# Kernel tuning notes

Measured on AMD Instinct MI355X. Metric: run time of the kernel, lower is better.

## Reference

```python
import jax, jax.numpy as jnp
import numpy as np

NHEAD = 8
LAYER_NAMES = ('self', 'cross', 'self', 'cross')
EPS = 1e-6


def ln(x, g, b, eps=1e-5):
    m = jnp.mean(x, -1, keepdims=True)
    v = jnp.mean((x - m) ** 2, -1, keepdims=True)
    return (x - m) * jax.lax.rsqrt(v + eps) * g + b


def linear_attention(q, k, v, q_mask, kv_mask):
    # q: [N, L, H, D], k/v: [N, S, H, D]; LoFTR LinearAttention (elu+1 feature map)
    Q = jax.nn.elu(q) + 1.0
    K = jax.nn.elu(k) + 1.0
    if q_mask is not None:
        Q = Q * q_mask[:, :, None, None].astype(Q.dtype)
    if kv_mask is not None:
        mk = kv_mask[:, :, None, None].astype(K.dtype)
        K = K * mk
        v = v * mk
    v_len = v.shape[1]
    v = v / v_len
    KV = jnp.einsum('nshd,nshv->nhdv', K, v)
    Z = 1.0 / (jnp.einsum('nlhd,nhd->nlh', Q, K.sum(1)) + EPS)
    return jnp.einsum('nlhd,nhdv,nlh->nlhv', Q, KV, Z) * v_len


def enc_layer(x, src, q_mask, kv_mask, Wq, Wk, Wv, Wm, W1, W2, g1, b1, g2, b2):
    # x: [N, L, C], src: [N, S, C]
    N, L, C = x.shape
    S = src.shape[1]
    H, D = NHEAD, C // NHEAD
    q = (x @ Wq).reshape(N, L, H, D)
    k = (src @ Wk).reshape(N, S, H, D)
    v = (src @ Wv).reshape(N, S, H, D)
    msg = linear_attention(q, k, v, q_mask, kv_mask).reshape(N, L, C)
    msg = ln(msg @ Wm, g1, b1)
    msg = ln(jnp.tanh(jnp.concatenate([x, msg], axis=-1) @ W1) @ W2, g2, b2)
    return x + msg


def sample_descriptors(kp, fmap, s):
    # kp: [B, L, K, 2] (x, y) raw-image pixel coords; fmap: [B, C, H, W]; s: stride
    B, C, H, W = fmap.shape
    k = kp - s / 2 + 0.5
    denom = jnp.array([W * s - s / 2 - 0.5, H * s - s / 2 - 0.5], dtype=kp.dtype)
    k = (k / denom) * 2.0 - 1.0  # normalized [-1, 1]
    px = (k[..., 0] + 1.0) * 0.5 * (W - 1)  # align_corners=True grid_sample
    py = (k[..., 1] + 1.0) * 0.5 * (H - 1)
    x0 = jnp.floor(px)
    y0 = jnp.floor(py)
    wx = (px - x0)[..., None]
    wy = (py - y0)[..., None]
    x0i = jnp.clip(x0, 0, W - 1).astype(jnp.int32)
    x1i = jnp.clip(x0 + 1, 0, W - 1).astype(jnp.int32)
    y0i = jnp.clip(y0, 0, H - 1).astype(jnp.int32)
    y1i = jnp.clip(y0 + 1, 0, H - 1).astype(jnp.int32)
    fm = jnp.transpose(fmap, (0, 2, 3, 1))  # [B, H, W, C]
    bidx = jnp.arange(B)[:, None, None]
    g00 = fm[bidx, y0i, x0i]
    g01 = fm[bidx, y0i, x1i]
    g10 = fm[bidx, y1i, x0i]
    g11 = fm[bidx, y1i, x1i]
    out = (1 - wy) * ((1 - wx) * g00 + wx * g01) + wy * ((1 - wx) * g10 + wx * g11)
    # SuperPoint-style L2 normalization of sampled descriptors
    out = out / (jnp.linalg.norm(out, axis=-1, keepdims=True) + 1e-8)
    return out  # [B, L, K, C]


def geo_transformer(feat0, feat1, kp0_cross, kp1_cross, mask_self0, mask_self1,
                    mask_cross0, mask_cross1, Wq, Wk, Wv, Wm, W1, W2, g1, b1, g2, b2,
                    h0, w0, h1, w1, scale):
    B, L0, C = feat0.shape
    L1 = feat1.shape[1]
    K = kp0_cross.shape[2]
    for i, name in enumerate(LAYER_NAMES):
        p = (Wq[i], Wk[i], Wv[i], Wm[i], W1[i], W2[i], g1[i], b1[i], g2[i], b2[i])
        if name == 'self':
            # source = masked subset of x == full source with kv-mask (v_length cancels)
            feat0 = enc_layer(feat0, feat0, None, mask_self0, *p)
            feat1 = enc_layer(feat1, feat1, None, mask_self1, *p)
        else:
            fmap0 = jnp.transpose(feat0.reshape(B, h0, w0, C), (0, 3, 1, 2))
            fmap1 = jnp.transpose(feat1.reshape(B, h1, w1, C), (0, 3, 1, 2))
            f0c = sample_descriptors(kp0_cross, fmap0, scale)  # [B, L1, K, C]
            f1c = sample_descriptors(kp1_cross, fmap1, scale)  # [B, L0, K, C]
            x0 = feat0.reshape(B * L0, 1, C)
            x1 = feat1.reshape(B * L1, 1, C)
            nf0 = enc_layer(x0, f1c.reshape(B * L0, K, C), None,
                            mask_cross1.reshape(B * L0, K), *p)
            nf1 = enc_layer(x1, f0c.reshape(B * L1, K, C), None,
                            mask_cross0.reshape(B * L1, K), *p)
            feat0 = nf0.reshape(B, L0, C)
            feat1 = nf1.reshape(B, L1, C)
    return feat0, feat1


def setup_inputs() -> dict:
    key = jax.random.key(0)
    B, H0, W0, C, K, S, NL = 2, 64, 64, 256, 9, 8, 4
    L = H0 * W0
    ks = jax.random.split(key, 16)
    std = (2.0 / (C + C)) ** 0.5
    std2 = (2.0 / (2 * C + 2 * C)) ** 0.5
    std3 = (2.0 / (2 * C + C)) ** 0.5
    kp0 = jnp.stack([
        jax.random.uniform(ks[2], (B, L, K)) * (W0 * S),
        jax.random.uniform(ks[3], (B, L, K)) * (H0 * S)], axis=-1)
    kp1 = jnp.stack([
        jax.random.uniform(ks[4], (B, L, K)) * (W0 * S),
        jax.random.uniform(ks[5], (B, L, K)) * (H0 * S)], axis=-1)
    return {
        'feat0': jax.random.normal(ks[0], (B, L, C), jnp.float32),
        'feat1': jax.random.normal(ks[1], (B, L, C), jnp.float32),
        'kp0_cross': kp0.astype(jnp.float32),
        'kp1_cross': kp1.astype(jnp.float32),
        'mask_self0': jax.random.bernoulli(ks[6], 0.9, (B, L)),
        'mask_self1': jax.random.bernoulli(ks[7], 0.9, (B, L)),
        'mask_cross0': jax.random.bernoulli(ks[8], 0.8, (B, L, K)),
        'mask_cross1': jax.random.bernoulli(ks[9], 0.8, (B, L, K)),
        'Wq': jax.random.normal(ks[10], (NL, C, C), jnp.float32) * std,
        'Wk': jax.random.normal(ks[11], (NL, C, C), jnp.float32) * std,
        'Wv': jax.random.normal(ks[12], (NL, C, C), jnp.float32) * std,
        'Wm': jax.random.normal(ks[13], (NL, C, C), jnp.float32) * std,
        'W1': jax.random.normal(ks[14], (NL, 2 * C, 2 * C), jnp.float32) * std2,
        'W2': jax.random.normal(ks[15], (NL, 2 * C, C), jnp.float32) * std3,
        'g1': jnp.ones((NL, C), jnp.float32),
        'b1': jnp.zeros((NL, C), jnp.float32),
        'g2': jnp.ones((NL, C), jnp.float32),
        'b2': jnp.zeros((NL, C), jnp.float32),
        'h0': H0, 'w0': W0, 'h1': H0, 'w1': W0, 'scale': S,
    }


def reference(feat0, feat1, kp0_cross, kp1_cross, mask_self0, mask_self1,
              mask_cross0, mask_cross1, Wq, Wk, Wv, Wm, W1, W2, g1, b1, g2, b2,
              h0, w0, h1, w1, scale):
    return geo_transformer(feat0, feat1, kp0_cross, kp1_cross, mask_self0, mask_self1,
                           mask_cross0, mask_cross1, Wq, Wk, Wv, Wm, W1, W2,
                           g1, b1, g2, b2, h0, w0, h1, w1, scale)
```

## Files before the change

### kernel.cpp

```cpp
#include <hip/hip_runtime.h>
#include <cstddef>


#define NROWS 16384

typedef unsigned short ushort_t;
typedef __attribute__((ext_vector_type(8))) short short8;
typedef __attribute__((ext_vector_type(4))) float f32x4;
typedef __attribute__((ext_vector_type(4))) unsigned short ushort4_t;
typedef __attribute__((ext_vector_type(8))) unsigned short ushort8_t;
typedef _Float16 half_t;
typedef __attribute__((ext_vector_type(4))) _Float16 half4;
typedef __attribute__((ext_vector_type(8))) _Float16 half8;

__device__ __forceinline__ float b2f(unsigned short u) {
    union { unsigned int i; float f; } v; v.i = (unsigned int)u << 16; return v.f;
}
__device__ __forceinline__ unsigned short f2b(float x) {
    union { float f; unsigned int i; } v; v.f = x;
    unsigned int r = v.i + 0x7fffu + ((v.i >> 16) & 1u);
    return (unsigned short)(r >> 16);
}
__device__ __forceinline__ ushort_t f2h(float x) {
    union { half_t h; ushort_t u; } v; v.h = (half_t)x; return v.u;
}
__device__ __forceinline__ float elu1(float x) {
    return x > 0.f ? x + 1.f : __expf(x);
}

#define ASYNC_COPY16(gptr, lptr) \
    __builtin_amdgcn_global_load_lds((const __attribute__((address_space(1))) void*)(gptr), \
                                     (__attribute__((address_space(3))) void*)(lptr), 16, 0, 0)

__global__ __launch_bounds__(256) void gemm_bf16_kernel(
    const ushort_t* __restrict__ A0, int lda0,
    const ushort_t* __restrict__ Wt, int ldw,
    ushort_t* __restrict__ C, int ldc, int Kd,
    float* __restrict__ zbuf, int znf4)
{
    __shared__ ushort_t As[128 * 64];
    __shared__ ushort_t Bs[128 * 64];

    int tid = threadIdx.x;
    int m0 = blockIdx.y * 128;
    int n0 = blockIdx.x * 128;
    int lane = tid & 63, w = tid >> 6;
    int wrow = w >> 1, wcol = w & 1;
    int quad = lane >> 4, l16 = lane & 15;

    if (zbuf && blockIdx.y == 0) {
        int nblk = gridDim.x;
        for (int i = blockIdx.x * 256 + tid; i < znf4; i += nblk * 256)
            *(float4*)&zbuf[(size_t)i * 4] = (float4){0.f, 0.f, 0.f, 0.f};
    }

    f32x4 acc[4][4];
    #pragma unroll
    for (int i = 0; i < 4; i++)
        #pragma unroll
        for (int j = 0; j < 4; j++) acc[i][j] = (f32x4){0.f, 0.f, 0.f, 0.f};

    for (int kb = 0; kb < Kd; kb += 64) {
        #pragma unroll
        for (int q = 0; q < 4; q++) {
            int s = q * 256 + tid;
            int kk = s >> 9, p = s & 511;
            int row = p >> 2, c4 = p & 3;
            ASYNC_COPY16(A0 + (size_t)(m0 + row) * lda0 + kb + kk * 32 + c4 * 8,
                         (char*)As + s * 16);
        }
        #pragma unroll
        for (int q = 0; q < 4; q++) {
            int s = q * 256 + tid;
            int kk = s >> 9, p = s & 511;
            int row = p >> 2, c4 = p & 3;
            ASYNC_COPY16(Wt + (size_t)(n0 + row) * ldw + kb + kk * 32 + c4 * 8,
                         (char*)Bs + s * 16);
        }
        __syncthreads();

        #pragma unroll
        for (int kk = 0; kk < 2; kk++) {
            short8 af[4], bf[4];
            #pragma unroll
            for (int mt = 0; mt < 4; mt++)
                af[mt] = *(const short8*)&As[kk * 4096 + (wrow * 64 + mt * 16 + l16) * 32 + quad * 8];
            #pragma unroll
            for (int nt = 0; nt < 4; nt++)
                bf[nt] = *(const short8*)&Bs[kk * 4096 + (wcol * 64 + nt * 16 + l16) * 32 + quad * 8];
            #pragma unroll
            for (int mt = 0; mt < 4; mt++)
                #pragma unroll
                for (int nt = 0; nt < 4; nt++)
                    acc[mt][nt] = __builtin_amdgcn_mfma_f32_16x16x32_bf16(
                        af[mt], bf[nt], acc[mt][nt], 0, 0, 0);
        }
        __syncthreads();
    }

    #pragma unroll
    for (int mt = 0; mt < 4; mt++) {
        int row = m0 + wrow * 64 + mt * 16 + quad * 4;
        #pragma unroll
        for (int nt = 0; nt < 4; nt++) {
            int col = n0 + wcol * 64 + nt * 16 + l16;
            #pragma unroll
            for (int r = 0; r < 4; r++)
                C[(size_t)(row + r) * ldc + col] = f2h(acc[mt][nt][r]);
        }
    }
}

__global__ __launch_bounds__(256) void gemm_ln_kernel(
    const ushort_t* __restrict__ A, int lda,
    const ushort_t* __restrict__ Wt, int ldw, int Kd,
    const float* __restrict__ g, const float* __restrict__ bp,
    ushort_t* __restrict__ OutBf)
{
    __shared__ ushort_t As[32 * 64];
    __shared__ ushort_t Bs[256 * 64];
    __shared__ float rsum[4][32];
    __shared__ float rsq[4][32];

    int tid = threadIdx.x;
    int m0 = blockIdx.x * 32;
    int lane = tid & 63, w = tid >> 6;
    int quad = lane >> 4, l16 = lane & 15;

    f32x4 acc[2][4];
    #pragma unroll
    for (int i = 0; i < 2; i++)
        #pragma unroll
        for (int j = 0; j < 4; j++) acc[i][j] = (f32x4){0.f, 0.f, 0.f, 0.f};

    for (int kb = 0; kb < Kd; kb += 64) {
        {
            int s = tid;
            int kk = s >> 7, p = s & 127;
            int row = p >> 2, c4 = p & 3;
            ASYNC_COPY16(A + (size_t)(m0 + row) * lda + kb + kk * 32 + c4 * 8,
                         (char*)As + s * 16);
        }
        #pragma unroll
        for (int q = 0; q < 8; q++) {
            int s = q * 256 + tid;
            int kk = s >> 10, p = s & 1023;
            int row = p >> 2, c4 = p & 3;
            ASYNC_COPY16(Wt + (size_t)(row) * ldw + kb + kk * 32 + c4 * 8,
                         (char*)Bs + s * 16);
        }
        __syncthreads();

        #pragma unroll
        for (int kk = 0; kk < 2; kk++) {
            short8 af[2], bf[4];
            #pragma unroll
            for (int mt = 0; mt < 2; mt++)
                af[mt] = *(const short8*)&As[kk * 1024 + (mt * 16 + l16) * 32 + quad * 8];
            #pragma unroll
            for (int nt = 0; nt < 4; nt++)
                bf[nt] = *(const short8*)&Bs[kk * 8192 + (w * 64 + nt * 16 + l16) * 32 + quad * 8];
            #pragma unroll
            for (int mt = 0; mt < 2; mt++)
                #pragma unroll
                for (int nt = 0; nt < 4; nt++)
                    acc[mt][nt] = __builtin_amdgcn_mfma_f32_16x16x32_bf16(
                        af[mt], bf[nt], acc[mt][nt], 0, 0, 0);
        }
        __syncthreads();
    }

    #pragma unroll
    for (int mt = 0; mt < 2; mt++)
        #pragma unroll
        for (int r = 0; r < 4; r++) {
            float s = 0.f, q = 0.f;
            #pragma unroll
            for (int nt = 0; nt < 4; nt++) {
                float v = acc[mt][nt][r];
                s += v; q += v * v;
            }
            #pragma unroll
            for (int off = 1; off < 16; off <<= 1) {
                s += __shfl_xor(s, off, 64);
                q += __shfl_xor(q, off, 64);
            }
            if (l16 == 0) {
                rsum[w][mt * 16 + quad * 4 + r] = s;
                rsq[w][mt * 16 + quad * 4 + r]  = q;
            }
        }
    __syncthreads();

    #pragma unroll
    for (int mt = 0; mt < 2; mt++) {
        #pragma unroll
        for (int r = 0; r < 4; r++) {
            int rl = mt * 16 + quad * 4 + r;
            float s = rsum[0][rl] + rsum[1][rl] + rsum[2][rl] + rsum[3][rl];
            float q = rsq[0][rl] + rsq[1][rl] + rsq[2][rl] + rsq[3][rl];
            float m = s * (1.f / 256.f);
            float var = q * (1.f / 256.f) - m * m;
            float rs = rsqrtf(var + 1e-5f);
            size_t row = (size_t)(m0 + rl);
            #pragma unroll
            for (int nt = 0; nt < 4; nt++) {
                int col = w * 64 + nt * 16 + l16;
                float y = (acc[mt][nt][r] - m) * rs * g[col] + bp[col];
                OutBf[row * 256 + col] = f2b(y);
            }
        }
    }
}

__global__ __launch_bounds__(256) void mlp_fused_kernel(
    const ushort_t* __restrict__ Xb, const ushort_t* __restrict__ L1,
    const ushort_t* __restrict__ W1t, const ushort_t* __restrict__ W2t,
    const float* __restrict__ g, const float* __restrict__ bp,
    ushort_t* __restrict__ XbfOut, const float* __restrict__ Xin,
    float* __restrict__ Xout)
{
    __shared__ ushort_t Tt[32 * 512];
    __shared__ char buf[20480];

    ushort_t* As  = (ushort_t*)buf;
    ushort_t* Bs  = (ushort_t*)(buf + 4096);
    ushort_t* Bs2 = (ushort_t*)buf;
    float* rsum = (float*)buf;
    float* rsq  = (float*)(buf + 512);

    int tid = threadIdx.x;
    int m0 = blockIdx.x * 32;
    int lane = tid & 63, w = tid >> 6;
    int quad = lane >> 4, l16 = lane & 15;

    for (int np = 0; np < 4; np++) {
        f32x4 acc[2][2];
        #pragma unroll
        for (int i = 0; i < 2; i++)
            #pragma unroll
            for (int j = 0; j < 2; j++) acc[i][j] = (f32x4){0.f, 0.f, 0.f, 0.f};

        for (int kb = 0; kb < 512; kb += 64) {
            const ushort_t* Ab = (kb < 256) ? Xb : L1;
            int kc = (kb < 256) ? kb : kb - 256;
            {
                int s = tid;
                int kk = s >> 7, p = s & 127;
                ASYNC_COPY16(Ab + (size_t)(m0 + (p >> 2)) * 256 + kc + kk * 32 + (p & 3) * 8,
                             (char*)As + s * 16);
            }
            #pragma unroll
            for (int q = 0; q < 4; q++) {
                int s = q * 256 + tid;
                int kk = s >> 9, p = s & 511;
                ASYNC_COPY16(W1t + (size_t)(np * 128 + (p >> 2)) * 512 + kb + kk * 32 + (p & 3) * 8,
                             (char*)Bs + s * 16);
            }
            __syncthreads();

            #pragma unroll
            for (int kk = 0; kk < 2; kk++) {
                short8 af[2], bfr[2];
                #pragma unroll
                for (int mt = 0; mt < 2; mt++)
                    af[mt] = *(const short8*)&As[kk * 1024 + (mt * 16 + l16) * 32 + quad * 8];
                #pragma unroll
                for (int nt = 0; nt < 2; nt++)
                    bfr[nt] = *(const short8*)&Bs[kk * 4096 + (w * 32 + nt * 16 + l16) * 32 + quad * 8];
                #pragma unroll
                for (int mt = 0; mt < 2; mt++)
                    #pragma unroll
                    for (int nt = 0; nt < 2; nt++)
                        acc[mt][nt] = __builtin_amdgcn_mfma_f32_16x16x32_bf16(
                            af[mt], bfr[nt], acc[mt][nt], 0, 0, 0);
            }
            __syncthreads();
        }

        #pragma unroll
        for (int mt = 0; mt < 2; mt++)
            #pragma unroll
            for (int nt = 0; nt < 2; nt++)
                #pragma unroll
                for (int r = 0; r < 4; r++) {
                    int trow = mt * 16 + quad * 4 + r;
                    int col = np * 128 + w * 32 + nt * 16 + l16;
                    int c8s = (col >> 3) ^ (trow & 7);
                    Tt[trow * 512 + c8s * 8 + (col & 7)] = f2b(tanhf(acc[mt][nt][r]));
                }
    }

    f32x4 acc2[2][2][2];
    #pragma unroll
    for (int a = 0; a < 2; a++)
        #pragma unroll
        for (int i = 0; i < 2; i++)
            #pragma unroll
            for (int j = 0; j < 2; j++) acc2[a][i][j] = (f32x4){0.f, 0.f, 0.f, 0.f};

    for (int pass = 0; pass < 2; pass++) {
        for (int kb = 0; kb < 512; kb += 64) {
            #pragma unroll
            for (int q = 0; q < 4; q++) {
                int s = q * 256 + tid;
                int kk = s >> 9, p = s & 511;
                ASYNC_COPY16(W2t + (size_t)(pass * 128 + (p >> 2)) * 512 + kb + kk * 32 + (p & 3) * 8,
                             (char*)Bs2 + s * 16);
            }
            __syncthreads();

            #pragma unroll
            for (int kk = 0; kk < 2; kk++) {
                short8 af[2], bfr[2];
                #pragma unroll
                for (int mt = 0; mt < 2; mt++) {
                    int row = mt * 16 + l16;
                    int blk = ((kb >> 3) + kk * 4 + quad) ^ (row & 7);
                    af[mt] = *(const short8*)&Tt[row * 512 + blk * 8];
                }
                #pragma unroll
                for (int nt = 0; nt < 2; nt++)
                    bfr[nt] = *(const short8*)&Bs2[kk * 4096 + (w * 32 + nt * 16 + l16) * 32 + quad * 8];
                #pragma unroll
                for (int mt = 0; mt < 2; mt++)
                    #pragma unroll
                    for (int nt = 0; nt < 2; nt++)
                        acc2[pass][mt][nt] = __builtin_amdgcn_mfma_f32_16x16x32_bf16(
                            af[mt], bfr[nt], acc2[pass][mt][nt], 0, 0, 0);
            }
            __syncthreads();
        }
    }

    #pragma unroll
    for (int mt = 0; mt < 2; mt++)
        #pragma unroll
        for (int r = 0; r < 4; r++) {
            float s = 0.f, q = 0.f;
            #pragma unroll
            for (int pass = 0; pass < 2; pass++)
                #pragma unroll
                for (int nt = 0; nt < 2; nt++) {
                    float v = acc2[pass][mt][nt][r];
                    s += v; q += v * v;
                }
            #pragma unroll
            for (int off = 1; off < 16; off <<= 1) {
                s += __shfl_xor(s, off, 64);
                q += __shfl_xor(q, off, 64);
            }
            if (l16 == 0) {
                rsum[w * 32 + mt * 16 + quad * 4 + r] = s;
                rsq[w * 32 + mt * 16 + quad * 4 + r]  = q;
            }
        }
    __syncthreads();

    #pragma unroll
    for (int mt = 0; mt < 2; mt++) {
        #pragma unroll
        for (int r = 0; r < 4; r++) {
            int rl = mt * 16 + quad * 4 + r;
            float s = rsum[rl] + rsum[32 + rl] + rsum[64 + rl] + rsum[96 + rl];
            float q = rsq[rl] + rsq[32 + rl] + rsq[64 + rl] + rsq[96 + rl];
            float m = s * (1.f / 256.f);
            float var = q * (1.f / 256.f) - m * m;
            float rs = rsqrtf(var + 1e-5f);
            size_t row = (size_t)(m0 + rl);
            #pragma unroll
            for (int pass = 0; pass < 2; pass++)
                #pragma unroll
                for (int nt = 0; nt < 2; nt++) {
                    int col = pass * 128 + w * 32 + nt * 16 + l16;
                    float y = (acc2[pass][mt][nt][r] - m) * rs * g[col] + bp[col];
                    float xn = Xin[row * 256 + col] + y;
                    Xout[row * 256 + col] = xn;
                    XbfOut[row * 256 + col] = f2b(xn);
                }
        }
    }
}

__global__ __launch_bounds__(256) void wprep_kernel(
    const float* __restrict__ Wq, const float* __restrict__ Wk,
    const float* __restrict__ Wv, const float* __restrict__ Wm,
    const float* __restrict__ W1, const float* __restrict__ W2,
    ushort_t* __restrict__ Wqkvt, ushort_t* __restrict__ Wmt,
    ushort_t* __restrict__ W1t, ushort_t* __restrict__ W2t)
{
    int t = blockIdx.x;
    int layer = t / 640, r = t % 640;
    const float* src; ushort_t* dst;
    int ldsrc, lddst, tn, tk;
    if (r < 192) {
        int grp = r / 64, rr = r % 64; tn = rr / 8; tk = rr % 8;
        src = (grp == 0 ? Wq : grp == 1 ? Wk : Wv) + (size_t)layer * 65536;
        ldsrc = 256;
        dst = Wqkvt + (size_t)layer * 196608 + (size_t)grp * 65536;
        lddst = 256;
    } else if (r < 256) {
        int rr = r - 192; tn = rr / 8; tk = rr % 8;
        src = Wm + (size_t)layer * 65536; ldsrc = 256;
        dst = Wmt + (size_t)layer * 65536; lddst = 256;
    } else if (r < 512) {
        int rr = r - 256; tn = rr / 16; tk = rr % 16;
        src = W1 + (size_t)layer * 262144; ldsrc = 512;
        dst = W1t + (size_t)layer * 262144; lddst = 512;
    } else {
        int rr = r - 512; tn = rr / 16; tk = rr % 16;
        src = W2 + (size_t)layer * 131072; ldsrc = 256;
        dst = W2t + (size_t)layer * 131072; lddst = 512;
    }
    int n0 = tn * 32, k0 = tk * 32;
    __shared__ float tileS[32][33];
    int j = threadIdx.x & 31, i0 = threadIdx.x >> 5;
    #pragma unroll
    for (int p = 0; p < 4; p++) {
        int i = i0 + p * 8;
        tileS[i][j] = src[(size_t)(k0 + i) * ldsrc + n0 + j];
    }
    __syncthreads();
    #pragma unroll
    for (int p = 0; p < 4; p++) {
        int i = i0 + p * 8;
        dst[(size_t)(n0 + i) * lddst + k0 + j] = f2b(tileS[j][i]);
    }
}

__global__ __launch_bounds__(256) void init_kernel(
    const float* __restrict__ f0, const float* __restrict__ f1,
    float* __restrict__ X, ushort_t* __restrict__ Xbf)
{
    int idx = blockIdx.x * 256 + threadIdx.x;
    size_t e = (size_t)idx * 4;
    float4 v = (e < 2097152) ? *(const float4*)&f0[e] : *(const float4*)&f1[e - 2097152];
    *(float4*)&X[e] = v;
    ushort4_t u = { f2b(v.x), f2b(v.y), f2b(v.z), f2b(v.w) };
    *(ushort4_t*)&Xbf[e] = u;
}

__global__ __launch_bounds__(256) void kv_reduce_kernel(
    const ushort_t* __restrict__ QKV,
    const int* __restrict__ mask0, const int* __restrict__ mask1,
    float* __restrict__ KV, float* __restrict__ Ksum)
{
    int g = blockIdx.y;
    int t = g >> 4, b = (g >> 3) & 1, h = g & 7;
    const int* mask = t ? mask1 : mask0;
    int rowbase = t * 8192 + b * 4096;
    int s_begin = blockIdx.x * 256;

    __shared__ float sK[32][32];
    __shared__ float sV[32][32];

    int tid = threadIdx.x;
    int e  = tid & 31;
    int dq = tid >> 5;

    float acc[4] = {0.f, 0.f, 0.f, 0.f};
    float ks[4]  = {0.f, 0.f, 0.f, 0.f};

    for (int s0 = s_begin; s0 < s_begin + 256; s0 += 32) {
        #pragma unroll
        for (int q = 0; q < 2; q++) {
            int idx = tid + q * 256;
            int rl = idx >> 4;
            int part = idx & 15;
            int s = s0 + rl;
            size_t row = (size_t)(rowbase + s);
            float m = mask[b * 4096 + s] ? 1.f : 0.f;
            if (part < 8) {
                half4 u = *(const half4*)&QKV[row * 768 + 256 + h * 32 + part * 4];
                float4 f = { elu1((float)u[0]) * m, elu1((float)u[1]) * m,
                             elu1((float)u[2]) * m, elu1((float)u[3]) * m };
                *(float4*)&sK[rl][part * 4] = f;
            } else {
                half4 u = *(const half4*)&QKV[row * 768 + 512 + h * 32 + (part - 8) * 4];
                float4 f = { (float)u[0] * m, (float)u[1] * m,
                             (float)u[2] * m, (float)u[3] * m };
                *(float4*)&sV[rl][(part - 8) * 4] = f;
            }
        }
        __syncthreads();

        #pragma unroll
        for (int s = 0; s < 32; s++) {
            float4 kq = *(const float4*)&sK[s][dq * 4];
            float vv = sV[s][e];
            acc[0] += kq.x * vv;
            acc[1] += kq.y * vv;
            acc[2] += kq.z * vv;
            acc[3] += kq.w * vv;
            ks[0] += kq.x; ks[1] += kq.y; ks[2] += kq.z; ks[3] += kq.w;
        }
        __syncthreads();
    }

    #pragma unroll
    for (int j = 0; j < 4; j++)
        atomicAdd(&KV[(size_t)g * 1024 + (dq * 4 + j) * 32 + e], acc[j]);
    if (e == 0) {
        #pragma unroll
        for (int j = 0; j < 4; j++)
            atomicAdd(&Ksum[g * 32 + dq * 4 + j], ks[j]);
    }
}

__global__ __launch_bounds__(256) void attn_apply_kernel(
    const ushort_t* __restrict__ QKV, const float* __restrict__ KV,
    const float* __restrict__ Ksum, ushort_t* __restrict__ MSG)
{
    int row = blockIdx.x;
    int t = row >> 13, bb = (row >> 12) & 1;
    int gb = (t * 2 + bb) * 8;
    int c = threadIdx.x, h = c >> 5, e = c & 31;
    int g = gb + h;

    __shared__ float sQ[256];
    float qf = elu1((float)(*(const half_t*)&QKV[(size_t)row * 768 + c]));
    sQ[c] = qf;
    __syncthreads();

    float p = qf * Ksum[g * 32 + e];
    #pragma unroll
    for (int off = 16; off; off >>= 1) p += __shfl_xor(p, off, 32);
    float Z = 1.f / (p + 1e-6f);

// ... 86 lines not shown
    float mU0, mU1, mU2, mU3, mSm;
    int mPack;
    {
        int msi = l32 % 5;
        int s9 = half + 2 * msi;
        int valid = (s9 < 9);
        int r = bl * 9 + (valid ? s9 : 0);
        mSm = (valid && mask[r] != 0) ? 1.f : 0.f;

        float2 xy = *(const float2*)&kp[(size_t)r * 2];
        float px = (xy.x - 3.5f) * (63.f / 507.5f);
        float py = (xy.y - 3.5f) * (63.f / 507.5f);
        float fx = floorf(px), fy = floorf(py);
        float wx = px - fx, wy = py - fy;
        int ix = (int)fx, iy = (int)fy;
        int xa = ix > 0 ? ix : 0;
        int xb = ix + 1 > 0 ? (ix + 1 < 63 ? ix + 1 : 63) : 0;
        int ya = iy > 0 ? iy : 0;
        int yb = iy + 1 > 0 ? (iy + 1 < 63 ? iy + 1 : 63) : 0;

        float w0 = (1.f - wy) * (1.f - wx);
        float w1 = (1.f - wy) * wx;
        float w2 = wy * (1.f - wx);
        float w3 = wy * wx;

        const float* G = &Gimg[(size_t)((iy + 1) * 65 + (ix + 1)) * 12];
        float4 ga = *(const float4*)&G[0];
        float4 gb4 = *(const float4*)&G[4];
        float2 gc = *(const float2*)&G[8];
        float ss = w0 * w0 * ga.x + w1 * w1 * gb4.x + w2 * w2 * gb4.w + w3 * w3 * gc.y
                 + 2.f * (w0 * w1 * ga.y + w0 * w2 * ga.z + w0 * w3 * ga.w
                        + w1 * w2 * gb4.y + w1 * w3 * gb4.z + w2 * w3 * gc.x);
        float inv = 1.f / (sqrtf(ss) + 1e-8f);
        mU0 = w0 * inv; mU1 = w1 * inv; mU2 = w2 * inv; mU3 = w3 * inv;

        int base = (rb + ya * 64 + xa) * 768;
        mPack = base | (xb - xa) | ((yb - ya) << 1);
    }

    int spack[5];
    float su0[5], su1[5], su2[5], su3[5], sm[5];
    int srcb = half * 32;
    #pragma unroll
    for (int si = 0; si < 5; si++) {
        int src = srcb + si;
        spack[si] = __shfl(mPack, src, 64);
        su0[si] = __shfl(mU0, src, 64);
        su1[si] = __shfl(mU1, src, 64);
        su2[si] = __shfl(mU2, src, 64);
        su3[si] = __shfl(mU3, src, 64);
        sm[si]  = __shfl(mSm, src, 64);
    }

    half8 kR[2][4], vR[2][4];

#define LOADKV(bufi, si_) do { \
        int pk = spack[si_]; \
        int dx = (pk & 1) ? 768 : 0; \
        int dy = (pk & 2) ? 49152 : 0; \
        size_t bK = (size_t)(pk & ~3) + 256 + c8; \
        size_t bV = bK + 256; \
        kR[bufi][0] = *(const half8*)&QKV[bK]; \
        kR[bufi][1] = *(const half8*)&QKV[bK + dx]; \
        kR[bufi][2] = *(const half8*)&QKV[bK + dy]; \
        kR[bufi][3] = *(const half8*)&QKV[bK + dx + dy]; \
        vR[bufi][0] = *(const half8*)&QKV[bV]; \
        vR[bufi][1] = *(const half8*)&QKV[bV + dx]; \
        vR[bufi][2] = *(const half8*)&QKV[bV + dy]; \
        vR[bufi][3] = *(const half8*)&QKV[bV + dx + dy]; \
    } while (0)

    float zsum = 0.f;
    float acc[8] = {0, 0, 0, 0, 0, 0, 0, 0};

    LOADKV(0, 0);
    #pragma unroll
    for (int si = 0; si < 5; si++) {
        int cur = si & 1;
        if (si + 1 < 5) {
            if (cur == 0) LOADKV(1, si + 1);
            else          LOADKV(0, si + 1);
        }
        float u0 = su0[si], u1 = su1[si], u2 = su2[si], u3 = su3[si];
        float p = 0.f;
        #pragma unroll
        for (int j = 0; j < 8; j++) {
            float kc = u0 * (float)kR[cur][0][j] + u1 * (float)kR[cur][1][j]
                     + u2 * (float)kR[cur][2][j] + u3 * (float)kR[cur][3][j];
            p += qf[j] * elu1(kc);
        }
        p += __shfl_xor(p, 1, 64);
        p += __shfl_xor(p, 2, 64);
        p *= sm[si];

        zsum += p;
        float pu0 = p * u0, pu1 = p * u1, pu2 = p * u2, pu3 = p * u3;
        #pragma unroll
        for (int j = 0; j < 8; j++)
            acc[j] += pu0 * (float)vR[cur][0][j] + pu1 * (float)vR[cur][1][j]
                    + pu2 * (float)vR[cur][2][j] + pu3 * (float)vR[cur][3][j];
    }
#undef LOADKV

    zsum += __shfl_xor(zsum, 32, 64);
    #pragma unroll
    for (int j = 0; j < 8; j++) acc[j] += __shfl_xor(acc[j], 32, 64);

    if (half == 0) {
        float Z = 1.f / (zsum + 1e-6f);
        ushort8_t o;
        #pragma unroll
        for (int j = 0; j < 8; j++) o[j] = f2b(acc[j] * Z);
        *(ushort8_t*)&MSG[(size_t)row * 256 + c8] = o;
    }
}


extern "C" void kernel_launch(void* const* d_in, const int* in_sizes, int n_in,
                              void* d_out, int out_size, void* d_ws, size_t ws_size,
                              hipStream_t stream)
{
    const float* feat0 = (const float*)d_in[0];
    const float* feat1 = (const float*)d_in[1];
    const float* kp0 = (const float*)d_in[2];
    const float* kp1 = (const float*)d_in[3];
    const int* ms0 = (const int*)d_in[4];
    const int* ms1 = (const int*)d_in[5];
    const int* mc0 = (const int*)d_in[6];
    const int* mc1 = (const int*)d_in[7];
    const float* Wq = (const float*)d_in[8];
    const float* Wk = (const float*)d_in[9];
    const float* Wv = (const float*)d_in[10];
    const float* Wm = (const float*)d_in[11];
    const float* W1 = (const float*)d_in[12];
    const float* W2 = (const float*)d_in[13];
    const float* g1 = (const float*)d_in[14];
    const float* b1 = (const float*)d_in[15];
    const float* g2 = (const float*)d_in[16];
    const float* b2 = (const float*)d_in[17];

    char* p = (char*)d_ws;
    float*    X     = (float*)p;            p += 16777216;
    ushort_t* Xbf   = (ushort_t*)p;         p += 8388608;
    ushort_t* QKV   = (ushort_t*)p;         p += 25165824;
    ushort_t* MSG   = (ushort_t*)p;         p += 8388608;
    ushort_t* L1bf  = (ushort_t*)p;         p += 8388608;
    float*    KVb   = (float*)p;            p += 131072;
    float*    KSb   = (float*)p;            p += 4096;
    float*    Gm    = (float*)p;            p += 811264;
    ushort_t* Wqkvt = (ushort_t*)p;         p += 1572864;
    ushort_t* Wmt   = (ushort_t*)p;         p += 524288;
    ushort_t* W1t   = (ushort_t*)p;         p += 2097152;
    ushort_t* W2t   = (ushort_t*)p;         p += 1048576;

    init_kernel<<<4096, 256, 0, stream>>>(feat0, feat1, X, Xbf);
    wprep_kernel<<<2560, 256, 0, stream>>>(Wq, Wk, Wv, Wm, W1, W2, Wqkvt, Wmt, W1t, W2t);

    for (int i = 0; i < 4; i++) {
        const ushort_t* Wqkvt_l = Wqkvt + (size_t)i * 196608;
        const ushort_t* Wmt_l   = Wmt   + (size_t)i * 65536;
        const ushort_t* W1t_l   = W1t   + (size_t)i * 262144;
        const ushort_t* W2t_l   = W2t   + (size_t)i * 131072;
        const float* g1_l = g1 + (size_t)i * 256;
        const float* b1_l = b1 + (size_t)i * 256;
        const float* g2_l = g2 + (size_t)i * 256;
        const float* b2_l = b2 + (size_t)i * 256;
        bool is_self = (i == 0 || i == 2);

        gemm_bf16_kernel<<<dim3(6, 128), 256, 0, stream>>>(
            Xbf, 256, Wqkvt_l, 256, QKV, 768, 256,
            is_self ? KVb : nullptr, 33792 / 4);

        if (is_self) {
            kv_reduce_kernel<<<dim3(16, 32), 256, 0, stream>>>(QKV, ms0, ms1, KVb, KSb);
            attn_apply_kernel<<<NROWS, 256, 0, stream>>>(QKV, KVb, KSb, MSG);
        } else {
            gram_kernel<<<4225, 256, 0, stream>>>(Xbf, Gm);
            cross_fused_kernel<<<NROWS / 4, 256, 0, stream>>>(QKV, Gm, kp0, kp1, mc0, mc1, MSG);
        }

        gemm_ln_kernel<<<NROWS / 32, 256, 0, stream>>>(
            MSG, 256, Wmt_l, 256, 256, g1_l, b1_l, L1bf);

        float* Xout = (i == 3) ? (float*)d_out : X;
        mlp_fused_kernel<<<NROWS / 32, 256, 0, stream>>>(
            Xbf, L1bf, W1t_l, W2t_l, g2_l, b2_l, Xbf, X, Xout);
    }
}
```

Before: 597.0 us.

## Load GEMM operands directly from global into registers, dropping LDS staging

In gemm_ln_kernel and mlp_fused_kernel, the async-copy LDS staging of the A and weight tiles is replaced by direct per-lane short8 global loads that feed the MFMA instructions. The per-iteration __syncthreads pairs go away, and in the MLP the four column passes are merged into one K loop with 32 accumulators, so each activation fragment is loaded once. The aim is to cut LDS traffic and barrier stalls and to improve occupancy through lower shared-memory use. In exchange it relies on L1/L2 for weight reuse across waves, raises register pressure, and hard-codes K=256 in gemm_ln.

```diff
diff --git a/kernel.cpp b/kernel.cpp
--- a/kernel.cpp
+++ b/kernel.cpp
@@ -117,8 +117,6 @@
     const float* __restrict__ g, const float* __restrict__ bp,
     ushort_t* __restrict__ OutBf)
 {
-    __shared__ ushort_t As[32 * 64];
-    __shared__ ushort_t Bs[256 * 64];
     __shared__ float rsum[4][32];
     __shared__ float rsq[4][32];
 
@@ -133,41 +131,24 @@
         #pragma unroll
         for (int j = 0; j < 4; j++) acc[i][j] = (f32x4){0.f, 0.f, 0.f, 0.f};
 
-    for (int kb = 0; kb < Kd; kb += 64) {
-        {
-            int s = tid;
-            int kk = s >> 7, p = s & 127;
-            int row = p >> 2, c4 = p & 3;
-            ASYNC_COPY16(A + (size_t)(m0 + row) * lda + kb + kk * 32 + c4 * 8,
-                         (char*)As + s * 16);
-        }
-        #pragma unroll
-        for (int q = 0; q < 8; q++) {
-            int s = q * 256 + tid;
-            int kk = s >> 10, p = s & 1023;
-            int row = p >> 2, c4 = p & 3;
-            ASYNC_COPY16(Wt + (size_t)(row) * ldw + kb + kk * 32 + c4 * 8,
-                         (char*)Bs + s * 16);
-        }
-        __syncthreads();
-
-        #pragma unroll
-        for (int kk = 0; kk < 2; kk++) {
-            short8 af[2], bf[4];
-            #pragma unroll
-            for (int mt = 0; mt < 2; mt++)
-                af[mt] = *(const short8*)&As[kk * 1024 + (mt * 16 + l16) * 32 + quad * 8];
+    const ushort_t* Ar0 = A + (size_t)(m0 + l16) * lda + quad * 8;
+    const ushort_t* Ar1 = Ar0 + (size_t)16 * lda;
+    const ushort_t* Br  = Wt + (size_t)(w * 64 + l16) * ldw + quad * 8;
+
+    #pragma unroll
+    for (int kb = 0; kb < 256; kb += 32) {
+        short8 af[2], bf[4];
+        af[0] = *(const short8*)(Ar0 + kb);
+        af[1] = *(const short8*)(Ar1 + kb);
+        #pragma unroll
+        for (int nt = 0; nt < 4; nt++)
+            bf[nt] = *(const short8*)(Br + (size_t)nt * 16 * ldw + kb);
+        #pragma unroll
+        for (int mt = 0; mt < 2; mt++)
             #pragma unroll
             for (int nt = 0; nt < 4; nt++)
-                bf[nt] = *(const short8*)&Bs[kk * 8192 + (w * 64 + nt * 16 + l16) * 32 + quad * 8];
-            #pragma unroll
-            for (int mt = 0; mt < 2; mt++)
-                #pragma unroll
-                for (int nt = 0; nt < 4; nt++)
-                    acc[mt][nt] = __builtin_amdgcn_mfma_f32_16x16x32_bf16(
-                        af[mt], bf[nt], acc[mt][nt], 0, 0, 0);
-        }
-        __syncthreads();
+                acc[mt][nt] = __builtin_amdgcn_mfma_f32_16x16x32_bf16(
+                    af[mt], bf[nt], acc[mt][nt], 0, 0, 0);
     }
 
     #pragma unroll
@@ -221,63 +202,54 @@
     float* __restrict__ Xout)
 {
     __shared__ ushort_t Tt[32 * 512];
-    __shared__ char buf[20480];
-
-    ushort_t* As  = (ushort_t*)buf;
-    ushort_t* Bs  = (ushort_t*)(buf + 4096);
-    ushort_t* Bs2 = (ushort_t*)buf;
-    float* rsum = (float*)buf;
-    float* rsq  = (float*)(buf + 512);
+    __shared__ float rsum[128];
+    __shared__ float rsq[128];
 
     int tid = threadIdx.x;
     int m0 = blockIdx.x * 32;
     int lane = tid & 63, w = tid >> 6;
     int quad = lane >> 4, l16 = lane & 15;
 
-    for (int np = 0; np < 4; np++) {
-        f32x4 acc[2][2];
+    f32x4 acc1[4][2][2];
+    #pragma unroll
+    for (int np = 0; np < 4; np++)
         #pragma unroll
         for (int i = 0; i < 2; i++)
             #pragma unroll
-            for (int j = 0; j < 2; j++) acc[i][j] = (f32x4){0.f, 0.f, 0.f, 0.f};
-
-        for (int kb = 0; kb < 512; kb += 64) {
-            const ushort_t* Ab = (kb < 256) ? Xb : L1;
-            int kc = (kb < 256) ? kb : kb - 256;
-            {
-                int s = tid;
-                int kk = s >> 7, p = s & 127;
-                ASYNC_COPY16(Ab + (size_t)(m0 + (p >> 2)) * 256 + kc + kk * 32 + (p & 3) * 8,
-                             (char*)As + s * 16);
-            }
-            #pragma unroll
-            for (int q = 0; q < 4; q++) {
-                int s = q * 256 + tid;
-                int kk = s >> 9, p = s & 511;
-                ASYNC_COPY16(W1t + (size_t)(np * 128 + (p >> 2)) * 512 + kb + kk * 32 + (p & 3) * 8,
-                             (char*)Bs + s * 16);
-            }
-            __syncthreads();
-
-            #pragma unroll
-            for (int kk = 0; kk < 2; kk++) {
-                short8 af[2], bfr[2];
+            for (int j = 0; j < 2; j++) acc1[np][i][j] = (f32x4){0.f, 0.f, 0.f, 0.f};
+
+    {
+        const ushort_t* Xr0 = Xb + (size_t)(m0 + l16) * 256 + quad * 8;
+        const ushort_t* Xr1 = Xr0 + 16 * 256;
+        const ushort_t* Lr0 = L1 + (size_t)(m0 + l16) * 256 + quad * 8;
+        const ushort_t* Lr1 = Lr0 + 16 * 256;
+        const ushort_t* B1  = W1t + (size_t)(w * 32 + l16) * 512 + quad * 8;
+
+        #pragma unroll
+        for (int kb = 0; kb < 512; kb += 32) {
+            short8 af[2];
+            if (kb < 256) {
+                af[0] = *(const short8*)(Xr0 + kb);
+                af[1] = *(const short8*)(Xr1 + kb);
+            } else {
+                af[0] = *(const short8*)(Lr0 + (kb - 256));
+                af[1] = *(const short8*)(Lr1 + (kb - 256));
+            }
+            #pragma unroll
+            for (int np = 0; np < 4; np++)
                 #pragma unroll
-                for (int mt = 0; mt < 2; mt++)
-                    af[mt] = *(const short8*)&As[kk * 1024 + (mt * 16 + l16) * 32 + quad * 8];
-                #pragma unroll
-                for (int nt = 0; nt < 2; nt++)
-                    bfr[nt] = *(const short8*)&Bs[kk * 4096 + (w * 32 + nt * 16 + l16) * 32 + quad * 8];
-                #pragma unroll
-                for (int mt = 0; mt < 2; mt++)
+                for (int nt = 0; nt < 2; nt++) {
+                    short8 b = *(const short8*)(B1 + (size_t)(np * 128 + nt * 16) * 512 + kb);
                     #pragma unroll
-                    for (int nt = 0; nt < 2; nt++)
-                        acc[mt][nt] = __builtin_amdgcn_mfma_f32_16x16x32_bf16(
-                            af[mt], bfr[nt], acc[mt][nt], 0, 0, 0);
-            }
-            __syncthreads();
-        }
-
+                    for (int mt = 0; mt < 2; mt++)
+                        acc1[np][mt][nt] = __builtin_amdgcn_mfma_f32_16x16x32_bf16(
+                            af[mt], b, acc1[np][mt][nt], 0, 0, 0);
+                }
+        }
+    }
+
+    #pragma unroll
+    for (int np = 0; np < 4; np++)
         #pragma unroll
         for (int mt = 0; mt < 2; mt++)
             #pragma unroll
@@ -287,9 +259,9 @@
                     int trow = mt * 16 + quad * 4 + r;
                     int col = np * 128 + w * 32 + nt * 16 + l16;
                     int c8s = (col >> 3) ^ (trow & 7);
-                    Tt[trow * 512 + c8s * 8 + (col & 7)] = f2b(tanhf(acc[mt][nt][r]));
+                    Tt[trow * 512 + c8s * 8 + (col & 7)] = f2b(tanhf(acc1[np][mt][nt][r]));
                 }
-    }
+    __syncthreads();
 
     f32x4 acc2[2][2][2];
     #pragma unroll
@@ -299,37 +271,28 @@
             #pragma unroll
             for (int j = 0; j < 2; j++) acc2[a][i][j] = (f32x4){0.f, 0.f, 0.f, 0.f};
 
-    for (int pass = 0; pass < 2; pass++) {
-        for (int kb = 0; kb < 512; kb += 64) {
-            #pragma unroll
-            for (int q = 0; q < 4; q++) {
-                int s = q * 256 + tid;
-                int kk = s >> 9, p = s & 511;
-                ASYNC_COPY16(W2t + (size_t)(pass * 128 + (p >> 2)) * 512 + kb + kk * 32 + (p & 3) * 8,
-                             (char*)Bs2 + s * 16);
-            }
-            __syncthreads();
-
-            #pragma unroll
-            for (int kk = 0; kk < 2; kk++) {
-                short8 af[2], bfr[2];
+    {
+        const ushort_t* B2 = W2t + (size_t)(w * 32 + l16) * 512 + quad * 8;
+
+        #pragma unroll
+        for (int kb = 0; kb < 512; kb += 32) {
+            short8 af[2];
+            #pragma unroll
+            for (int mt = 0; mt < 2; mt++) {
+                int row = mt * 16 + l16;
+                int blk = ((kb >> 3) + quad) ^ (row & 7);
+                af[mt] = *(const short8*)&Tt[row * 512 + blk * 8];
+            }
+            #pragma unroll
+            for (int pass = 0; pass < 2; pass++)
                 #pragma unroll
-                for (int mt = 0; mt < 2; mt++) {
-                    int row = mt * 16 + l16;
-                    int blk = ((kb >> 3) + kk * 4 + quad) ^ (row & 7);
-                    af[mt] = *(const short8*)&Tt[row * 512 + blk * 8];
+                for (int nt = 0; nt < 2; nt++) {
+                    short8 b = *(const short8*)(B2 + (size_t)(pass * 128 + nt * 16) * 512 + kb);
+                    #pragma unroll
+                    for (int mt = 0; mt < 2; mt++)
+                        acc2[pass][mt][nt] = __builtin_amdgcn_mfma_f32_16x16x32_bf16(
+                            af[mt], b, acc2[pass][mt][nt], 0, 0, 0);
                 }
-                #pragma unroll
-                for (int nt = 0; nt < 2; nt++)
-                    bfr[nt] = *(const short8*)&Bs2[kk * 4096 + (w * 32 + nt * 16 + l16) * 32 + quad * 8];
-                #pragma unroll
-                for (int mt = 0; mt < 2; mt++)
-                    #pragma unroll
-                    for (int nt = 0; nt < 2; nt++)
-                        acc2[pass][mt][nt] = __builtin_amdgcn_mfma_f32_16x16x32_bf16(
-                            af[mt], bfr[nt], acc2[pass][mt][nt], 0, 0, 0);
-            }
-            __syncthreads();
         }
     }
 
```

Result: slower. 760.0 us (+27.3%).

## Fuse merge-projection LayerNorm GEMM into the MLP kernel with shared-memory intermediates

Applied to the files above, without the earlier changes.

Merges the Wm GEMM+LayerNorm kernel into the MLP kernel, so the first LayerNorm output and the block's input rows stay in swizzled shared memory instead of going through global memory. The MLP is also restructured to interleave W1 and W2 per 128-column chunk, keeping only a 32x128 tanh tile rather than the full 32x512 intermediate. This removes one launch and the L1bf global write/read. The cost is more shared memory per block, which may lower occupancy, and W2 tiles are now reloaded in smaller K chunks across the four np iterations.

```diff
diff --git a/kernel.cpp b/kernel.cpp
--- a/kernel.cpp
+++ b/kernel.cpp
@@ -111,42 +111,54 @@
     }
 }
 
-__global__ __launch_bounds__(256) void gemm_ln_kernel(
-    const ushort_t* __restrict__ A, int lda,
-    const ushort_t* __restrict__ Wt, int ldw, int Kd,
-    const float* __restrict__ g, const float* __restrict__ bp,
-    ushort_t* __restrict__ OutBf)
-{
+__global__ __launch_bounds__(256) void mlp_ln_fused_kernel(
+    const ushort_t* __restrict__ MSG, const ushort_t* __restrict__ Wmt,
+    const float* __restrict__ g1, const float* __restrict__ b1,
+    const ushort_t* __restrict__ Xb,
+    const ushort_t* __restrict__ W1t, const ushort_t* __restrict__ W2t,
+    const float* __restrict__ g2, const float* __restrict__ bp,
+    ushort_t* __restrict__ XbfOut, const float* __restrict__ Xin,
+    float* __restrict__ Xout)
+{
+    __shared__ ushort_t XB[32 * 256];
+    __shared__ ushort_t L1s[32 * 256];
+    __shared__ ushort_t Tnp[32 * 128];
+    __shared__ ushort_t Bs[256 * 64];
     __shared__ ushort_t As[32 * 64];
-    __shared__ ushort_t Bs[256 * 64];
-    __shared__ float rsum[4][32];
-    __shared__ float rsq[4][32];
+    __shared__ float stats[256];
 
     int tid = threadIdx.x;
     int m0 = blockIdx.x * 32;
     int lane = tid & 63, w = tid >> 6;
     int quad = lane >> 4, l16 = lane & 15;
 
-    f32x4 acc[2][4];
+    #pragma unroll
+    for (int i = 0; i < 4; i++) {
+        int s = i * 256 + tid;
+        int row = s >> 5, gp = s & 31;
+        int gsrc = gp ^ (row & 7);
+        ASYNC_COPY16(Xb + (size_t)(m0 + row) * 256 + gsrc * 8,
+                     (char*)XB + s * 16);
+    }
+
+    f32x4 accA[2][4];
     #pragma unroll
     for (int i = 0; i < 2; i++)
         #pragma unroll
-        for (int j = 0; j < 4; j++) acc[i][j] = (f32x4){0.f, 0.f, 0.f, 0.f};
-
-    for (int kb = 0; kb < Kd; kb += 64) {
+        for (int j = 0; j < 4; j++) accA[i][j] = (f32x4){0.f, 0.f, 0.f, 0.f};
+
+    for (int kb = 0; kb < 256; kb += 64) {
         {
             int s = tid;
             int kk = s >> 7, p = s & 127;
-            int row = p >> 2, c4 = p & 3;
-            ASYNC_COPY16(A + (size_t)(m0 + row) * lda + kb + kk * 32 + c4 * 8,
+            ASYNC_COPY16(MSG + (size_t)(m0 + (p >> 2)) * 256 + kb + kk * 32 + (p & 3) * 8,
                          (char*)As + s * 16);
         }
         #pragma unroll
         for (int q = 0; q < 8; q++) {
             int s = q * 256 + tid;
             int kk = s >> 10, p = s & 1023;
-            int row = p >> 2, c4 = p & 3;
-            ASYNC_COPY16(Wt + (size_t)(row) * ldw + kb + kk * 32 + c4 * 8,
+            ASYNC_COPY16(Wmt + (size_t)(p >> 2) * 256 + kb + kk * 32 + (p & 3) * 8,
                          (char*)Bs + s * 16);
         }
         __syncthreads();
@@ -164,8 +176,8 @@
             for (int mt = 0; mt < 2; mt++)
                 #pragma unroll
                 for (int nt = 0; nt < 4; nt++)
-                    acc[mt][nt] = __builtin_amdgcn_mfma_f32_16x16x32_bf16(
-                        af[mt], bf[nt], acc[mt][nt], 0, 0, 0);
+                    accA[mt][nt] = __builtin_amdgcn_mfma_f32_16x16x32_bf16(
+                        af[mt], bf[nt], accA[mt][nt], 0, 0, 0);
         }
         __syncthreads();
     }
@@ -177,7 +189,7 @@
             float s = 0.f, q = 0.f;
             #pragma unroll
             for (int nt = 0; nt < 4; nt++) {
-                float v = acc[mt][nt][r];
+                float v = accA[mt][nt][r];
                 s += v; q += v * v;
             }
             #pragma unroll
@@ -186,8 +198,8 @@
                 q += __shfl_xor(q, off, 64);
             }
             if (l16 == 0) {
-                rsum[w][mt * 16 + quad * 4 + r] = s;
-                rsq[w][mt * 16 + quad * 4 + r]  = q;
+                stats[w * 32 + mt * 16 + quad * 4 + r] = s;
+                stats[128 + w * 32 + mt * 16 + quad * 4 + r] = q;
             }
         }
     __syncthreads();
@@ -197,183 +209,163 @@
         #pragma unroll
         for (int r = 0; r < 4; r++) {
             int rl = mt * 16 + quad * 4 + r;
-            float s = rsum[0][rl] + rsum[1][rl] + rsum[2][rl] + rsum[3][rl];
-            float q = rsq[0][rl] + rsq[1][rl] + rsq[2][rl] + rsq[3][rl];
+            float s = stats[rl] + stats[32 + rl] + stats[64 + rl] + stats[96 + rl];
+            float q = stats[128 + rl] + stats[160 + rl] + stats[192 + rl] + stats[224 + rl];
+            float m = s * (1.f / 256.f);
+            float var = q * (1.f / 256.f) - m * m;
+            float rs = rsqrtf(var + 1e-5f);
+            #pragma unroll
+            for (int nt = 0; nt < 4; nt++) {
+                int col = w * 64 + nt * 16 + l16;
+                float y = (accA[mt][nt][r] - m) * rs * g1[col] + b1[col];
+                L1s[rl * 256 + (((col >> 3) ^ (rl & 7)) << 3) + (col & 7)] = f2b(y);
+            }
+        }
+    }
+    __syncthreads();
+
+    f32x4 acc2[2][2][2];
+    #pragma unroll
+    for (int a = 0; a < 2; a++)
+        #pragma unroll
+        for (int i = 0; i < 2; i++)
+            #pragma unroll
+            for (int j = 0; j < 2; j++) acc2[a][i][j] = (f32x4){0.f, 0.f, 0.f, 0.f};
+
+    #pragma unroll
+    for (int np = 0; np < 4; np++) {
+        f32x4 acc1[2][2];
+        #pragma unroll
+        for (int i = 0; i < 2; i++)
+            #pragma unroll
+            for (int j = 0; j < 2; j++) acc1[i][j] = (f32x4){0.f, 0.f, 0.f, 0.f};
+
+        #pragma unroll
+        for (int kb = 0; kb < 512; kb += 128) {
+            #pragma unroll
+            for (int q = 0; q < 8; q++) {
+                int s = q * 256 + tid;
+                int kk = s >> 9, p = s & 511;
+                ASYNC_COPY16(W1t + (size_t)(np * 128 + (p >> 2)) * 512 + kb + kk * 32 + (p & 3) * 8,
+                             (char*)Bs + s * 16);
+            }
+            __syncthreads();
+
+            #pragma unroll
+            for (int kk = 0; kk < 4; kk++) {
+                short8 af[2], bfr[2];
+                #pragma unroll
+                for (int mt = 0; mt < 2; mt++) {
+                    int row = mt * 16 + l16;
+                    int k = kb + kk * 32 + quad * 8;
+                    if (k < 256)
+                        af[mt] = *(const short8*)&XB[row * 256 + (((k >> 3) ^ (row & 7)) << 3)];
+                    else
+                        af[mt] = *(const short8*)&L1s[row * 256 + ((((k - 256) >> 3) ^ (row & 7)) << 3)];
+                }
+                #pragma unroll
+                for (int nt = 0; nt < 2; nt++)
+                    bfr[nt] = *(const short8*)&Bs[kk * 4096 + (w * 32 + nt * 16 + l16) * 32 + quad * 8];
+                #pragma unroll
+                for (int mt = 0; mt < 2; mt++)
+                    #pragma unroll
+                    for (int nt = 0; nt < 2; nt++)
+                        acc1[mt][nt] = __builtin_amdgcn_mfma_f32_16x16x32_bf16(
+                            af[mt], bfr[nt], acc1[mt][nt], 0, 0, 0);
+            }
+            __syncthreads();
+        }
+
+        #pragma unroll
+        for (int mt = 0; mt < 2; mt++)
+            #pragma unroll
+            for (int nt = 0; nt < 2; nt++)
+                #pragma unroll
+                for (int r = 0; r < 4; r++) {
+                    int trow = mt * 16 + quad * 4 + r;
+                    int c = w * 32 + nt * 16 + l16;
+                    Tnp[trow * 128 + (((c >> 3) ^ (trow & 7)) << 3) + (c & 7)] =
+                        f2b(tanhf(acc1[mt][nt][r]));
+                }
+        __syncthreads();
+
+        #pragma unroll
+        for (int kb2 = 0; kb2 < 128; kb2 += 64) {
+            #pragma unroll
+            for (int q = 0; q < 8; q++) {
+                int s = q * 256 + tid;
+                int kk = s >> 10, p = s & 1023;
+                ASYNC_COPY16(W2t + (size_t)(p >> 2) * 512 + np * 128 + kb2 + kk * 32 + (p & 3) * 8,
+                             (char*)Bs + s * 16);
+            }
+            __syncthreads();
+
+            #pragma unroll
+            for (int kk = 0; kk < 2; kk++) {
+                short8 af[2];
+                #pragma unroll
+                for (int mt = 0; mt < 2; mt++) {
+                    int row = mt * 16 + l16;
+                    int klocal = kb2 + kk * 32 + quad * 8;
+                    af[mt] = *(const short8*)&Tnp[row * 128 + (((klocal >> 3) ^ (row & 7)) << 3)];
+                }
+                #pragma unroll
+                for (int pass = 0; pass < 2; pass++)
+                    #pragma unroll
+                    for (int nt = 0; nt < 2; nt++) {
+                        short8 bfr = *(const short8*)&Bs[kk * 8192 +
+                            (pass * 128 + w * 32 + nt * 16 + l16) * 32 + quad * 8];
+                        #pragma unroll
+                        for (int mt = 0; mt < 2; mt++)
+                            acc2[pass][mt][nt] = __builtin_amdgcn_mfma_f32_16x16x32_bf16(
+                                af[mt], bfr, acc2[pass][mt][nt], 0, 0, 0);
+                    }
+            }
+            __syncthreads();
+        }
+    }
+
+    #pragma unroll
+    for (int mt = 0; mt < 2; mt++)
+        #pragma unroll
+        for (int r = 0; r < 4; r++) {
+            float s = 0.f, q = 0.f;
+            #pragma unroll
+            for (int pass = 0; pass < 2; pass++)
+                #pragma unroll
+                for (int nt = 0; nt < 2; nt++) {
+                    float v = acc2[pass][mt][nt][r];
+                    s += v; q += v * v;
+                }
+            #pragma unroll
+            for (int off = 1; off < 16; off <<= 1) {
+                s += __shfl_xor(s, off, 64);
+                q += __shfl_xor(q, off, 64);
+            }
+            if (l16 == 0) {
+                stats[w * 32 + mt * 16 + quad * 4 + r] = s;
+                stats[128 + w * 32 + mt * 16 + quad * 4 + r] = q;
+            }
+        }
+    __syncthreads();
+
+    #pragma unroll
+    for (int mt = 0; mt < 2; mt++) {
+        #pragma unroll
+        for (int r = 0; r < 4; r++) {
+            int rl = mt * 16 + quad * 4 + r;
+            float s = stats[rl] + stats[32 + rl] + stats[64 + rl] + stats[96 + rl];
+            float q = stats[128 + rl] + stats[160 + rl] + stats[192 + rl] + stats[224 + rl];
             float m = s * (1.f / 256.f);
             float var = q * (1.f / 256.f) - m * m;
             float rs = rsqrtf(var + 1e-5f);
             size_t row = (size_t)(m0 + rl);
             #pragma unroll
-            for (int nt = 0; nt < 4; nt++) {
-                int col = w * 64 + nt * 16 + l16;
-                float y = (acc[mt][nt][r] - m) * rs * g[col] + bp[col];
-                OutBf[row * 256 + col] = f2b(y);
-            }
-        }
-    }
-}
-
-__global__ __launch_bounds__(256) void mlp_fused_kernel(
-    const ushort_t* __restrict__ Xb, const ushort_t* __restrict__ L1,
-    const ushort_t* __restrict__ W1t, const ushort_t* __restrict__ W2t,
-    const float* __restrict__ g, const float* __restrict__ bp,
-    ushort_t* __restrict__ XbfOut, const float* __restrict__ Xin,
-    float* __restrict__ Xout)
-{
-    __shared__ ushort_t Tt[32 * 512];
-    __shared__ char buf[20480];
-
-    ushort_t* As  = (ushort_t*)buf;
-    ushort_t* Bs  = (ushort_t*)(buf + 4096);
-    ushort_t* Bs2 = (ushort_t*)buf;
-    float* rsum = (float*)buf;
-    float* rsq  = (float*)(buf + 512);
-
-    int tid = threadIdx.x;
-    int m0 = blockIdx.x * 32;
-    int lane = tid & 63, w = tid >> 6;
-    int quad = lane >> 4, l16 = lane & 15;
-
-    for (int np = 0; np < 4; np++) {
-        f32x4 acc[2][2];
-        #pragma unroll
-        for (int i = 0; i < 2; i++)
-            #pragma unroll
-            for (int j = 0; j < 2; j++) acc[i][j] = (f32x4){0.f, 0.f, 0.f, 0.f};
-
-        for (int kb = 0; kb < 512; kb += 64) {
-            const ushort_t* Ab = (kb < 256) ? Xb : L1;
-            int kc = (kb < 256) ? kb : kb - 256;
-            {
-                int s = tid;
-                int kk = s >> 7, p = s & 127;
-                ASYNC_COPY16(Ab + (size_t)(m0 + (p >> 2)) * 256 + kc + kk * 32 + (p & 3) * 8,
-                             (char*)As + s * 16);
-            }
-            #pragma unroll
-            for (int q = 0; q < 4; q++) {
-                int s = q * 256 + tid;
-                int kk = s >> 9, p = s & 511;
-                ASYNC_COPY16(W1t + (size_t)(np * 128 + (p >> 2)) * 512 + kb + kk * 32 + (p & 3) * 8,
-                             (char*)Bs + s * 16);
-            }
-            __syncthreads();
-
-            #pragma unroll
-            for (int kk = 0; kk < 2; kk++) {
-                short8 af[2], bfr[2];
-                #pragma unroll
-                for (int mt = 0; mt < 2; mt++)
-                    af[mt] = *(const short8*)&As[kk * 1024 + (mt * 16 + l16) * 32 + quad * 8];
-                #pragma unroll
-                for (int nt = 0; nt < 2; nt++)
-                    bfr[nt] = *(const short8*)&Bs[kk * 4096 + (w * 32 + nt * 16 + l16) * 32 + quad * 8];
-                #pragma unroll
-                for (int mt = 0; mt < 2; mt++)
-                    #pragma unroll
-                    for (int nt = 0; nt < 2; nt++)
-                        acc[mt][nt] = __builtin_amdgcn_mfma_f32_16x16x32_bf16(
-                            af[mt], bfr[nt], acc[mt][nt], 0, 0, 0);
-            }
-            __syncthreads();
-        }
-
-        #pragma unroll
-        for (int mt = 0; mt < 2; mt++)
-            #pragma unroll
-            for (int nt = 0; nt < 2; nt++)
-                #pragma unroll
-                for (int r = 0; r < 4; r++) {
-                    int trow = mt * 16 + quad * 4 + r;
-                    int col = np * 128 + w * 32 + nt * 16 + l16;
-                    int c8s = (col >> 3) ^ (trow & 7);
-                    Tt[trow * 512 + c8s * 8 + (col & 7)] = f2b(tanhf(acc[mt][nt][r]));
-                }
-    }
-
-    f32x4 acc2[2][2][2];
-    #pragma unroll
-    for (int a = 0; a < 2; a++)
-        #pragma unroll
-        for (int i = 0; i < 2; i++)
-            #pragma unroll
-            for (int j = 0; j < 2; j++) acc2[a][i][j] = (f32x4){0.f, 0.f, 0.f, 0.f};
-
-    for (int pass = 0; pass < 2; pass++) {
-        for (int kb = 0; kb < 512; kb += 64) {
-            #pragma unroll
-            for (int q = 0; q < 4; q++) {
-                int s = q * 256 + tid;
-                int kk = s >> 9, p = s & 511;
-                ASYNC_COPY16(W2t + (size_t)(pass * 128 + (p >> 2)) * 512 + kb + kk * 32 + (p & 3) * 8,
-                             (char*)Bs2 + s * 16);
-            }
-            __syncthreads();
-
-            #pragma unroll
-            for (int kk = 0; kk < 2; kk++) {
-                short8 af[2], bfr[2];
-                #pragma unroll
-                for (int mt = 0; mt < 2; mt++) {
-                    int row = mt * 16 + l16;
-                    int blk = ((kb >> 3) + kk * 4 + quad) ^ (row & 7);
-                    af[mt] = *(const short8*)&Tt[row * 512 + blk * 8];
-                }
-                #pragma unroll
-                for (int nt = 0; nt < 2; nt++)
-                    bfr[nt] = *(const short8*)&Bs2[kk * 4096 + (w * 32 + nt * 16 + l16) * 32 + quad * 8];
-                #pragma unroll
-                for (int mt = 0; mt < 2; mt++)
-                    #pragma unroll
-                    for (int nt = 0; nt < 2; nt++)
-                        acc2[pass][mt][nt] = __builtin_amdgcn_mfma_f32_16x16x32_bf16(
-                            af[mt], bfr[nt], acc2[pass][mt][nt], 0, 0, 0);
-            }
-            __syncthreads();
-        }
-    }
-
-    #pragma unroll
-    for (int mt = 0; mt < 2; mt++)
-        #pragma unroll
-        for (int r = 0; r < 4; r++) {
-            float s = 0.f, q = 0.f;
-            #pragma unroll
-            for (int pass = 0; pass < 2; pass++)
-                #pragma unroll
-                for (int nt = 0; nt < 2; nt++) {
-                    float v = acc2[pass][mt][nt][r];
-                    s += v; q += v * v;
-                }
-            #pragma unroll
-            for (int off = 1; off < 16; off <<= 1) {
-                s += __shfl_xor(s, off, 64);
-                q += __shfl_xor(q, off, 64);
-            }
-            if (l16 == 0) {
-                rsum[w * 32 + mt * 16 + quad * 4 + r] = s;
-                rsq[w * 32 + mt * 16 + quad * 4 + r]  = q;
-            }
-        }
-    __syncthreads();
-
-    #pragma unroll
-    for (int mt = 0; mt < 2; mt++) {
-        #pragma unroll
-        for (int r = 0; r < 4; r++) {
-            int rl = mt * 16 + quad * 4 + r;
-            float s = rsum[rl] + rsum[32 + rl] + rsum[64 + rl] + rsum[96 + rl];
-            float q = rsq[rl] + rsq[32 + rl] + rsq[64 + rl] + rsq[96 + rl];
-            float m = s * (1.f / 256.f);
-            float var = q * (1.f / 256.f) - m * m;
-            float rs = rsqrtf(var + 1e-5f);
-            size_t row = (size_t)(m0 + rl);
-            #pragma unroll
             for (int pass = 0; pass < 2; pass++)
                 #pragma unroll
                 for (int nt = 0; nt < 2; nt++) {
                     int col = pass * 128 + w * 32 + nt * 16 + l16;
-                    float y = (acc2[pass][mt][nt][r] - m) * rs * g[col] + bp[col];
+                    float y = (acc2[pass][mt][nt][r] - m) * rs * g2[col] + bp[col];
                     float xn = Xin[row * 256 + col] + y;
                     Xout[row * 256 + col] = xn;
                     XbfOut[row * 256 + col] = f2b(xn);
@@ -766,6 +758,7 @@
     ushort_t* Wmt   = (ushort_t*)p;         p += 524288;
     ushort_t* W1t   = (ushort_t*)p;         p += 2097152;
     ushort_t* W2t   = (ushort_t*)p;         p += 1048576;
+    (void)L1bf;
 
     init_kernel<<<4096, 256, 0, stream>>>(feat0, feat1, X, Xbf);
     wprep_kernel<<<2560, 256, 0, stream>>>(Wq, Wk, Wv, Wm, W1, W2, Wqkvt, Wmt, W1t, W2t);
@@ -793,11 +786,8 @@
             cross_fused_kernel<<<NROWS / 4, 256, 0, stream>>>(QKV, Gm, kp0, kp1, mc0, mc1, MSG);
         }
 
-        gemm_ln_kernel<<<NROWS / 32, 256, 0, stream>>>(
-            MSG, 256, Wmt_l, 256, 256, g1_l, b1_l, L1bf);
-
         float* Xout = (i == 3) ? (float*)d_out : X;
-        mlp_fused_kernel<<<NROWS / 32, 256, 0, stream>>>(
-            Xbf, L1bf, W1t_l, W2t_l, g2_l, b2_l, Xbf, X, Xout);
-    }
-}
+        mlp_ln_fused_kernel<<<NROWS / 32, 256, 0, stream>>>(
+            MSG, Wmt_l, g1_l, b1_l, Xbf, W1t_l, W2t_l, g2_l, b2_l, Xbf, X, Xout);
+    }
+}
```

Result: faster. 563.5 us (-5.6%).
